# Optimization experiments

Hardware: AMD Instinct MI355X
Metric: run time of the kernel (lower is better)

## Reference

```python
import jax, jax.numpy as jnp
import numpy as np

# Hardware / quantization constants (DacAdcHardwareSettings + quant scales)
INPUT_BITS = 8
OUT_PREC_BITS = 8          # fractional precision bits of the ADC
OUT_RANGE_BITS = 4         # ADC full-scale range = 2**OUT_RANGE_BITS
VMAX = 0.6                 # DAC output voltage full scale
OUT_SCALE = 8020.0         # hardware_output_current_scaling (current -> ADC units)
INPUT_FACTOR = 0.15        # 1/(activation scale * quant_max)
OUTPUT_FACTOR = 0.01       # weight scale * activation scale * quant_max
G_SCALE = 1e-4             # conductance magnitude (Siemens) for memristor cells
WEIGHT_PRECISION = 4       # -> 3 bit-plane memristor arrays


def dac(x):
    # clamp to [-1,1], quantize to INPUT_BITS signed levels, scale to volts
    levels = 2.0 ** (INPUT_BITS - 1) - 1.0
    return VMAX * jnp.round(jnp.clip(x, -1.0, 1.0) * levels) / levels


def adc(current):
    # scale current to ADC units, quantize with fixed fractional step, clip to range
    step = 2.0 ** (-OUT_PREC_BITS)
    rng = 2.0 ** OUT_RANGE_BITS
    scaled = current * OUT_SCALE
    return jnp.clip(jnp.round(scaled / step) * step, -rng, rng)


def setup_inputs() -> dict:
    key = jax.random.key(0)
    k0, k1, k2, k3 = jax.random.split(key, 4)
    tokens, d_in, d_out = 8192, 4096, 4096
    n_planes = WEIGHT_PRECISION - 1
    x = jax.random.normal(k0, (tokens, d_in), dtype=jnp.float32)
    # paired memristor conductances per bit plane, input-major [plane, in, out]
    w_pos = jax.random.uniform(k1, (n_planes, d_in, d_out), dtype=jnp.float32) * G_SCALE
    w_neg = jax.random.uniform(k2, (n_planes, d_in, d_out), dtype=jnp.float32) * G_SCALE
    bias = jax.random.normal(k3, (d_out,), dtype=jnp.float32)
    return {"x": x, "w_pos": w_pos, "w_neg": w_neg, "bias": bias}


def reference(x, w_pos, w_neg, bias):
    # DAC: quantize scaled activations to drive voltages
    inp = dac(x * INPUT_FACTOR)                      # [B, I]
    # effective bit-plane weights: positive minus negative cell conductances
    w_eff = w_pos - w_neg                            # [P, I, O]
    # crossbar readout for all bit planes: I = V @ G
    planes = jnp.einsum('bi,pio->pbo', inp, w_eff)   # [P, B, O]
    q = adc(planes)                                  # quantized per plane
    # shift-accumulate: memristors[-1] is bit 0; memristors[i] (i<P-2) is bit P-2-i
    p = w_eff.shape[0]
    shifts = jnp.array([2.0 ** (p - 1 - i) for i in range(p)],
                       dtype=x.dtype)
    shifts = shifts.at[-1].set(1.0)                  # [4., 2., 1.] for precision 4
    mem_out = jnp.einsum('pbo,p->bo', q, shifts)
    return mem_out * OUTPUT_FACTOR + bias
```

## Files before the change

kernel.cpp:

```cpp
#include <hip/hip_runtime.h>
#include <hip/hip_bf16.h>
#include <stdint.h>

#define TOK  8192
#define DIN  4096
#define DOUT 4096
#define NPL  3

typedef unsigned short u16;
typedef __attribute__((ext_vector_type(8))) __bf16 bf16x8;
typedef __attribute__((ext_vector_type(4))) float f32x4;
typedef __attribute__((ext_vector_type(4))) unsigned short u16x4;

#define ADC_MUL   9699.7795275590551f
#define INV256    0.00390625f

__device__ __forceinline__ void gload_lds16(const void* g, void* l) {
    __builtin_amdgcn_global_load_lds(
        (const __attribute__((address_space(1))) void*)g,
        (__attribute__((address_space(3))) void*)l, 16, 0, 0);
}

__global__ void dac_kernel(const float* __restrict__ x, u16* __restrict__ a) {
    const int n4 = TOK * DIN / 4;
    int i = blockIdx.x * blockDim.x + threadIdx.x;
    const int stride = gridDim.x * blockDim.x;
    const float4* xv = (const float4*)x;
    u16x4* av = (u16x4*)a;
    for (; i < n4; i += stride) {
        float4 v = xv[i];
        u16x4 o;
        float t, k;
        t = v.x * 0.15f; t = fminf(1.0f, fmaxf(-1.0f, t)); k = rintf(t * 127.0f);
        o.x = (u16)(__float_as_uint(k) >> 16);
        t = v.y * 0.15f; t = fminf(1.0f, fmaxf(-1.0f, t)); k = rintf(t * 127.0f);
        o.y = (u16)(__float_as_uint(k) >> 16);
        t = v.z * 0.15f; t = fminf(1.0f, fmaxf(-1.0f, t)); k = rintf(t * 127.0f);
        o.z = (u16)(__float_as_uint(k) >> 16);
        t = v.w * 0.15f; t = fminf(1.0f, fmaxf(-1.0f, t)); k = rintf(t * 127.0f);
        o.w = (u16)(__float_as_uint(k) >> 16);
        av[i] = o;
    }
}

__global__ void wsplit_kernel(const float* __restrict__ wp, const float* __restrict__ wn,
                              u16* __restrict__ whi, u16* __restrict__ wlo) {
    __shared__ float tile[64][65];
    const int b   = blockIdx.x;
    const int p   = b >> 12;
    const int rem = b & 4095;
    const int ib  = rem >> 6, ob = rem & 63;
    const size_t plane = (size_t)p * DIN * DOUT;
    const int tx = threadIdx.x & 63, ty = threadIdx.x >> 6;

#pragma unroll
    for (int r = ty; r < 64; r += 4) {
        size_t off = plane + (size_t)(ib * 64 + r) * DOUT + ob * 64 + tx;
        tile[r][tx] = wp[off] - wn[off];
    }
    __syncthreads();
#pragma unroll
    for (int r = ty; r < 64; r += 4) {
        float d = tile[tx][r];
        uint32_t db = __float_as_uint(d);
        uint32_t hb = (db + 0x7fffu + ((db >> 16) & 1u)) & 0xffff0000u;
        float hf = __uint_as_float(hb);
        float l  = d - hf;
        uint32_t lb = __float_as_uint(l);
        u16 lo16 = (u16)((lb + 0x7fffu + ((lb >> 16) & 1u)) >> 16);
        size_t off = plane + (size_t)(ob * 64 + r) * DIN + ib * 64 + tx;
        whi[off] = (u16)(hb >> 16);
        wlo[off] = lo16;
    }
}

__global__ __launch_bounds__(256, 2) void gemm_kernel(
    const u16* __restrict__ A,
    const u16* __restrict__ Whi,
    const u16* __restrict__ Wlo,
    const float* __restrict__ bias,
    float* __restrict__ out)
{
    __shared__ __align__(16) char lds[49152];
    char* sA = lds;
    char* sH = lds + 16384;
    char* sL = lds + 32768;

    const int bid  = blockIdx.x;
    const int swz  = ((bid & 7) << 8) | (bid >> 3);
    const int mblk = swz & 63, nblk = swz >> 6;
    const int row0 = mblk << 7, col0 = nblk << 7;

    const int tid  = threadIdx.x;
    const int lane = tid & 63, wid = tid >> 6;
    const int wm = wid & 1, wn = wid >> 1;

    const int rbase = tid >> 3;
    const int scb   = (((tid & 7) ^ ((tid >> 3) & 7)) << 4);
    const char* gA = (const char*)A;

    const int arow = (wm << 6) + (lane & 15);
    const int brow = (wn << 6) + (lane & 15);
    const int ksw  = (lane & 7) << 4;
    const int kb   = (lane >> 4) << 4;
    const int koff0 = kb ^ ksw;
    const int koff1 = (64 + kb) ^ ksw;

    f32x4 fin[4][4];
#pragma unroll
    for (int i = 0; i < 4; ++i)
#pragma unroll
        for (int j = 0; j < 4; ++j) fin[i][j] = (f32x4){0.f, 0.f, 0.f, 0.f};

    const float shifts[NPL] = {4.0f, 2.0f, 1.0f};

    for (int p = 0; p < NPL; ++p) {
        const char* baseH = (const char*)Whi + (size_t)p * DIN * DOUT * 2;
        const char* baseL = (const char*)Wlo + (size_t)p * DIN * DOUT * 2;

        f32x4 acc[4][4];
#pragma unroll
        for (int i = 0; i < 4; ++i)
#pragma unroll
            for (int j = 0; j < 4; ++j) acc[i][j] = (f32x4){0.f, 0.f, 0.f, 0.f};

        for (int kt = 0; kt < DIN / 64; ++kt) {
            const int kcb = kt << 7;
#pragma unroll
            for (int it = 0; it < 4; ++it) {
                const int r = (it << 5) + rbase;
                const int ldst = (it << 12) + (wid << 10);
                const size_t aoff = (size_t)(row0 + r) * (DIN * 2) + kcb + scb;
                gload_lds16(gA + aoff, sA + ldst);
                const size_t woff = (size_t)(col0 + r) * (DIN * 2) + kcb + scb;
                gload_lds16(baseH + woff, sH + ldst);
                gload_lds16(baseL + woff, sL + ldst);
            }
            __syncthreads();

#pragma unroll
            for (int ks = 0; ks < 2; ++ks) {
                const int ko = ks ? koff1 : koff0;
                bf16x8 av[4], hv[4], lv[4];
#pragma unroll
                for (int mi = 0; mi < 4; ++mi)
                    av[mi] = *(const bf16x8*)(sA + ((arow + (mi << 4)) << 7) + ko);
#pragma unroll
                for (int ni = 0; ni < 4; ++ni) {
                    hv[ni] = *(const bf16x8*)(sH + ((brow + (ni << 4)) << 7) + ko);
                    lv[ni] = *(const bf16x8*)(sL + ((brow + (ni << 4)) << 7) + ko);
                }
#pragma unroll
                for (int mi = 0; mi < 4; ++mi)
#pragma unroll
                    for (int ni = 0; ni < 4; ++ni) {
                        acc[mi][ni] = __builtin_amdgcn_mfma_f32_16x16x32_bf16(
                            av[mi], hv[ni], acc[mi][ni], 0, 0, 0);
                        acc[mi][ni] = __builtin_amdgcn_mfma_f32_16x16x32_bf16(
                            av[mi], lv[ni], acc[mi][ni], 0, 0, 0);
                    }
            }
            __syncthreads();
        }

        const float sh = shifts[p];
#pragma unroll
        for (int mi = 0; mi < 4; ++mi)
#pragma unroll
            for (int ni = 0; ni < 4; ++ni)
#pragma unroll
                for (int r = 0; r < 4; ++r) {
                    float q = rintf(acc[mi][ni][r] * ADC_MUL) * INV256;
                    q = fminf(16.0f, fmaxf(-16.0f, q));
                    fin[mi][ni][r] += sh * q;
                }
    }

    const int orow = row0 + (wm << 6) + ((lane >> 4) << 2);
    const int ocol = col0 + (wn << 6) + (lane & 15);
#pragma unroll
    for (int ni = 0; ni < 4; ++ni) {
        const int c = ocol + (ni << 4);
        const float bv = bias[c];
#pragma unroll
        for (int mi = 0; mi < 4; ++mi)
#pragma unroll
            for (int r = 0; r < 4; ++r)
                out[(size_t)(orow + (mi << 4) + r) * DOUT + c] = fin[mi][ni][r] * 0.01f + bv;
    }
}

extern "C" void kernel_launch(void* const* d_in, const int* in_sizes, int n_in,
                              void* d_out, int out_size, void* d_ws, size_t ws_size,
                              hipStream_t stream) {
    const float* x    = (const float*)d_in[0];
    const float* wp   = (const float*)d_in[1];
    const float* wn   = (const float*)d_in[2];
    const float* bias = (const float*)d_in[3];
    float* out = (float*)d_out;

    u16* A   = (u16*)d_ws;
    u16* Whi = A + (size_t)TOK * DIN;
    u16* Wlo = Whi + (size_t)NPL * DIN * DOUT;

    dac_kernel<<<dim3(4096), dim3(256), 0, stream>>>(x, A);
    wsplit_kernel<<<dim3(NPL * 64 * 64), dim3(256), 0, stream>>>(wp, wn, Whi, Wlo);
    gemm_kernel<<<dim3(2048), dim3(256), 0, stream>>>(A, Whi, Wlo, bias, out);
}
```

Baseline: 1.995 ms.

## Interleave bf16 hi/lo weight planes along K and triple-buffer the GEMM pipeline

The weight split now writes hi and lo bf16 halves of every plane into one interleaved K-major buffer (24576 per output column). The GEMM then runs a single K loop over 384 tiles, with the ADC quantisation applied every 128 tiles instead of separate per-plane loops. The GEMM tile grows to 256x128 with 512 threads, and a 3-stage LDS ring with split async loads replaces the load-sync-compute-sync pattern, with MFMA priority raised. The wsplit load side is vectorised to float4. The larger LDS footprint (144KB) caps occupancy at one block per CU, and the explicit vmcnt waits make the pipeline fragile if the load counts change.

```diff
diff --git a/kernel.cpp b/kernel.cpp
--- a/kernel.cpp
+++ b/kernel.cpp
@@ -15,11 +15,9 @@
 #define ADC_MUL   9699.7795275590551f
 #define INV256    0.00390625f
 
-__device__ __forceinline__ void gload_lds16(const void* g, void* l) {
-    __builtin_amdgcn_global_load_lds(
-        (const __attribute__((address_space(1))) void*)g,
-        (__attribute__((address_space(3))) void*)l, 16, 0, 0);
-}
+#define GL(src, dst) __builtin_amdgcn_global_load_lds( \
+    (const __attribute__((address_space(1))) void*)(src), \
+    (__attribute__((address_space(3))) void*)(dst), 16, 0, 0)
 
 __global__ void dac_kernel(const float* __restrict__ x, u16* __restrict__ a) {
     const int n4 = TOK * DIN / 4;
@@ -44,149 +42,167 @@
 }
 
 __global__ void wsplit_kernel(const float* __restrict__ wp, const float* __restrict__ wn,
-                              u16* __restrict__ whi, u16* __restrict__ wlo) {
+                              u16* __restrict__ w) {
     __shared__ float tile[64][65];
     const int b   = blockIdx.x;
     const int p   = b >> 12;
     const int rem = b & 4095;
     const int ib  = rem >> 6, ob = rem & 63;
+    const int t   = threadIdx.x;
     const size_t plane = (size_t)p * DIN * DOUT;
-    const int tx = threadIdx.x & 63, ty = threadIdx.x >> 6;
-
-#pragma unroll
-    for (int r = ty; r < 64; r += 4) {
-        size_t off = plane + (size_t)(ib * 64 + r) * DOUT + ob * 64 + tx;
-        tile[r][tx] = wp[off] - wn[off];
+
+    {
+        const int o4 = (t & 15) << 2;
+        const int r0 = t >> 4;
+#pragma unroll
+        for (int pass = 0; pass < 4; ++pass) {
+            const int r = (pass << 4) + r0;
+            const size_t off = plane + (size_t)(ib * 64 + r) * DOUT + ob * 64 + o4;
+            const float4 a = *(const float4*)(wp + off);
+            const float4 c = *(const float4*)(wn + off);
+            tile[r][o4 + 0] = a.x - c.x;
+            tile[r][o4 + 1] = a.y - c.y;
+            tile[r][o4 + 2] = a.z - c.z;
+            tile[r][o4 + 3] = a.w - c.w;
+        }
     }
     __syncthreads();
-#pragma unroll
-    for (int r = ty; r < 64; r += 4) {
-        float d = tile[tx][r];
+    const int lane = t & 63, w4 = t >> 6;
+#pragma unroll
+    for (int pass = 0; pass < 16; ++pass) {
+        const int o = (pass << 2) + w4;
+        float d = tile[lane][o];
         uint32_t db = __float_as_uint(d);
         uint32_t hb = (db + 0x7fffu + ((db >> 16) & 1u)) & 0xffff0000u;
-        float hf = __uint_as_float(hb);
-        float l  = d - hf;
+        float l = d - __uint_as_float(hb);
         uint32_t lb = __float_as_uint(l);
         u16 lo16 = (u16)((lb + 0x7fffu + ((lb >> 16) & 1u)) >> 16);
-        size_t off = plane + (size_t)(ob * 64 + r) * DIN + ib * 64 + tx;
-        whi[off] = (u16)(hb >> 16);
-        wlo[off] = lo16;
-    }
-}
-
-__global__ __launch_bounds__(256, 2) void gemm_kernel(
+        size_t base = (size_t)(ob * 64 + o) * 24576 + (size_t)p * 8192 + ib * 64 + lane;
+        w[base] = (u16)(hb >> 16);
+        w[base + 4096] = lo16;
+    }
+}
+
+__global__ __launch_bounds__(512, 2) void gemm_kernel(
     const u16* __restrict__ A,
-    const u16* __restrict__ Whi,
-    const u16* __restrict__ Wlo,
+    const u16* __restrict__ W,
     const float* __restrict__ bias,
     float* __restrict__ out)
 {
-    __shared__ __align__(16) char lds[49152];
-    char* sA = lds;
-    char* sH = lds + 16384;
-    char* sL = lds + 32768;
-
-    const int bid  = blockIdx.x;
-    const int swz  = ((bid & 7) << 8) | (bid >> 3);
-    const int mblk = swz & 63, nblk = swz >> 6;
-    const int row0 = mblk << 7, col0 = nblk << 7;
-
-    const int tid  = threadIdx.x;
+    __shared__ __align__(16) char lds[147456];
+
+    const int bid = blockIdx.x;
+    const int g   = ((bid & 7) << 7) | (bid >> 3);
+    const int mblk = g & 31, nblk = g >> 5;
+    const int row0 = mblk << 8, col0 = nblk << 7;
+
+    const int tid = threadIdx.x;
     const int lane = tid & 63, wid = tid >> 6;
-    const int wm = wid & 1, wn = wid >> 1;
-
-    const int rbase = tid >> 3;
-    const int scb   = (((tid & 7) ^ ((tid >> 3) & 7)) << 4);
+    const int wm = wid & 3, wn = wid >> 2;
+
+    const int swzb = (((tid & 7) ^ ((tid >> 3) & 7)) << 4);
     const char* gA = (const char*)A;
-
-    const int arow = (wm << 6) + (lane & 15);
-    const int brow = (wn << 6) + (lane & 15);
-    const int ksw  = (lane & 7) << 4;
-    const int kb   = (lane >> 4) << 4;
-    const int koff0 = kb ^ ksw;
-    const int koff1 = (64 + kb) ^ ksw;
-
-    f32x4 fin[4][4];
+    const char* gB = (const char*)W;
+    const size_t aRow = (size_t)(row0 + (tid >> 3)) * (DIN * 2) + swzb;
+    const size_t bRow = (size_t)(col0 + (tid >> 3)) * (24576 * 2) + swzb;
+    const int dstL = wid << 10;
+
+    const int offK0 = (((lane >> 4) + 0) ^ (lane & 7)) << 4;
+    const int offK1 = (((lane >> 4) + 4) ^ (lane & 7)) << 4;
+    const int aRdRow = ((wm << 6) + (lane & 15)) << 7;
+    const int bRdRow = ((wn << 6) + (lane & 15)) << 7;
+
+    f32x4 acc[4][4], fin[4][4];
 #pragma unroll
     for (int i = 0; i < 4; ++i)
 #pragma unroll
-        for (int j = 0; j < 4; ++j) fin[i][j] = (f32x4){0.f, 0.f, 0.f, 0.f};
-
-    const float shifts[NPL] = {4.0f, 2.0f, 1.0f};
-
-    for (int p = 0; p < NPL; ++p) {
-        const char* baseH = (const char*)Whi + (size_t)p * DIN * DOUT * 2;
-        const char* baseL = (const char*)Wlo + (size_t)p * DIN * DOUT * 2;
-
-        f32x4 acc[4][4];
-#pragma unroll
-        for (int i = 0; i < 4; ++i)
-#pragma unroll
-            for (int j = 0; j < 4; ++j) acc[i][j] = (f32x4){0.f, 0.f, 0.f, 0.f};
-
-        for (int kt = 0; kt < DIN / 64; ++kt) {
-            const int kcb = kt << 7;
-#pragma unroll
-            for (int it = 0; it < 4; ++it) {
-                const int r = (it << 5) + rbase;
-                const int ldst = (it << 12) + (wid << 10);
-                const size_t aoff = (size_t)(row0 + r) * (DIN * 2) + kcb + scb;
-                gload_lds16(gA + aoff, sA + ldst);
-                const size_t woff = (size_t)(col0 + r) * (DIN * 2) + kcb + scb;
-                gload_lds16(baseH + woff, sH + ldst);
-                gload_lds16(baseL + woff, sL + ldst);
-            }
-            __syncthreads();
-
-#pragma unroll
-            for (int ks = 0; ks < 2; ++ks) {
-                const int ko = ks ? koff1 : koff0;
-                bf16x8 av[4], hv[4], lv[4];
-#pragma unroll
-                for (int mi = 0; mi < 4; ++mi)
-                    av[mi] = *(const bf16x8*)(sA + ((arow + (mi << 4)) << 7) + ko);
-#pragma unroll
-                for (int ni = 0; ni < 4; ++ni) {
-                    hv[ni] = *(const bf16x8*)(sH + ((brow + (ni << 4)) << 7) + ko);
-                    lv[ni] = *(const bf16x8*)(sL + ((brow + (ni << 4)) << 7) + ko);
-                }
-#pragma unroll
-                for (int mi = 0; mi < 4; ++mi)
-#pragma unroll
-                    for (int ni = 0; ni < 4; ++ni) {
-                        acc[mi][ni] = __builtin_amdgcn_mfma_f32_16x16x32_bf16(
-                            av[mi], hv[ni], acc[mi][ni], 0, 0, 0);
-                        acc[mi][ni] = __builtin_amdgcn_mfma_f32_16x16x32_bf16(
-                            av[mi], lv[ni], acc[mi][ni], 0, 0, 0);
+        for (int j = 0; j < 4; ++j) {
+            acc[i][j] = (f32x4){0.f, 0.f, 0.f, 0.f};
+            fin[i][j] = (f32x4){0.f, 0.f, 0.f, 0.f};
+        }
+
+    auto stage = [&](int tile, int part, int buf) {
+        const size_t kB = (size_t)tile << 7;
+        const size_t kA = (size_t)((tile & 63) << 7);
+        char* la = lds + (buf << 15) + dstL;
+        char* lb = lds + 98304 + (buf << 14) + dstL;
+        if (part == 0) {
+            GL(gA + aRow + kA,           la);
+            GL(gA + aRow + kA + 524288,  la + 8192);
+            GL(gB + bRow + kB,           lb);
+        } else {
+            GL(gA + aRow + kA + 1048576, la + 16384);
+            GL(gA + aRow + kA + 1572864, la + 24576);
+            GL(gB + bRow + kB + 3145728, lb + 8192);
+        }
+    };
+
+    auto phase = [&](int aBuf, int bBuf, int offK, int stTile, int stPart, int stBuf,
+                     bool doStage) {
+        bf16x8 av[4], bv[4];
+        const char* la = lds + aBuf + aRdRow + offK;
+        const char* lb = lds + bBuf + bRdRow + offK;
+#pragma unroll
+        for (int mi = 0; mi < 4; ++mi) av[mi] = *(const bf16x8*)(la + (mi << 11));
+#pragma unroll
+        for (int ni = 0; ni < 4; ++ni) bv[ni] = *(const bf16x8*)(lb + (ni << 11));
+        if (doStage) stage(stTile, stPart, stBuf);
+        asm volatile("s_waitcnt lgkmcnt(0)" ::: "memory");
+        __builtin_amdgcn_sched_barrier(0);
+        __builtin_amdgcn_s_setprio(1);
+#pragma unroll
+        for (int mi = 0; mi < 4; ++mi)
+#pragma unroll
+            for (int ni = 0; ni < 4; ++ni)
+                acc[mi][ni] = __builtin_amdgcn_mfma_f32_16x16x32_bf16(
+                    av[mi], bv[ni], acc[mi][ni], 0, 0, 0);
+        __builtin_amdgcn_s_setprio(0);
+    };
+
+    stage(0, 0, 0); stage(0, 1, 0);
+    stage(1, 0, 1); stage(1, 1, 1);
+    asm volatile("s_waitcnt vmcnt(6)" ::: "memory");
+    __builtin_amdgcn_s_barrier();
+
+    int bufc = 0;
+    for (int kt = 0; kt < 384; ++kt) {
+        const int nxt  = bufc ? bufc - 1 : 2;
+        const int aBuf = bufc << 15;
+        const int bBuf = 98304 + (bufc << 14);
+        const bool st  = (kt < 382);
+        phase(aBuf, bBuf, offK0, kt + 2, 0, nxt, st);
+        phase(aBuf, bBuf, offK1, kt + 2, 1, nxt, st);
+        if ((kt & 127) == 127) {
+            const float sh = (kt < 128) ? 4.f : (kt < 256) ? 2.f : 1.f;
+#pragma unroll
+            for (int mi = 0; mi < 4; ++mi)
+#pragma unroll
+                for (int ni = 0; ni < 4; ++ni)
+#pragma unroll
+                    for (int r = 0; r < 4; ++r) {
+                        float q = rintf(acc[mi][ni][r] * ADC_MUL) * INV256;
+                        q = fminf(16.0f, fmaxf(-16.0f, q));
+                        fin[mi][ni][r] += sh * q;
+                        acc[mi][ni][r] = 0.f;
                     }
-            }
-            __syncthreads();
-        }
-
-        const float sh = shifts[p];
+        }
+        if (st) { asm volatile("s_waitcnt vmcnt(6)" ::: "memory"); }
+        else    { asm volatile("s_waitcnt vmcnt(0)" ::: "memory"); }
+        __builtin_amdgcn_s_barrier();
+        bufc = (bufc == 2) ? 0 : bufc + 1;
+    }
+
+    const int orow0 = row0 + (wm << 6) + ((lane >> 4) << 2);
+    const int ocol0 = col0 + (wn << 6) + (lane & 15);
+#pragma unroll
+    for (int ni = 0; ni < 4; ++ni) {
+        const int c = ocol0 + (ni << 4);
+        const float bv = bias[c];
 #pragma unroll
         for (int mi = 0; mi < 4; ++mi)
 #pragma unroll
-            for (int ni = 0; ni < 4; ++ni)
-#pragma unroll
-                for (int r = 0; r < 4; ++r) {
-                    float q = rintf(acc[mi][ni][r] * ADC_MUL) * INV256;
-                    q = fminf(16.0f, fmaxf(-16.0f, q));
-                    fin[mi][ni][r] += sh * q;
-                }
-    }
-
-    const int orow = row0 + (wm << 6) + ((lane >> 4) << 2);
-    const int ocol = col0 + (wn << 6) + (lane & 15);
-#pragma unroll
-    for (int ni = 0; ni < 4; ++ni) {
-        const int c = ocol + (ni << 4);
-        const float bv = bias[c];
-#pragma unroll
-        for (int mi = 0; mi < 4; ++mi)
-#pragma unroll
             for (int r = 0; r < 4; ++r)
-                out[(size_t)(orow + (mi << 4) + r) * DOUT + c] = fin[mi][ni][r] * 0.01f + bv;
+                out[(size_t)(orow0 + (mi << 4) + r) * DOUT + c] = fin[mi][ni][r] * 0.01f + bv;
     }
 }
 
@@ -199,11 +215,10 @@
     const float* bias = (const float*)d_in[3];
     float* out = (float*)d_out;
 
-    u16* A   = (u16*)d_ws;
-    u16* Whi = A + (size_t)TOK * DIN;
-    u16* Wlo = Whi + (size_t)NPL * DIN * DOUT;
+    u16* A = (u16*)d_ws;
+    u16* W = A + (size_t)TOK * DIN;
 
     dac_kernel<<<dim3(4096), dim3(256), 0, stream>>>(x, A);
-    wsplit_kernel<<<dim3(NPL * 64 * 64), dim3(256), 0, stream>>>(wp, wn, Whi, Wlo);
-    gemm_kernel<<<dim3(2048), dim3(256), 0, stream>>>(A, Whi, Wlo, bias, out);
-}
+    wsplit_kernel<<<dim3(NPL * 64 * 64), dim3(256), 0, stream>>>(wp, wn, W);
+    gemm_kernel<<<dim3(1024), dim3(512), 0, stream>>>(A, W, bias, out);
+}
```

New measurement: 2.267 ms. +13.7%, slower.
